# Kernel tuning notes

Hardware: AMD Instinct MI355X
Metric: run time of the kernel (lower is better)

Reference implementation:

```python
import jax, jax.numpy as jnp
import numpy as np


def setup_inputs() -> dict:
    key = jax.random.key(0)
    ks = jax.random.split(key, 5)
    B, S, H = 4, 4096, 512
    std = 1.0 / np.sqrt(H)
    x = jax.random.normal(ks[0], (B, S, H), dtype=jnp.float32)
    relative_pos = jax.random.normal(ks[1], (B, S, H), dtype=jnp.float32)
    Wq = jax.random.normal(ks[2], (H, H), dtype=jnp.float32) * std
    Wk = jax.random.normal(ks[3], (H, H), dtype=jnp.float32) * std
    Wv = jax.random.normal(ks[4], (H, H), dtype=jnp.float32) * std
    bq = jnp.zeros((H,), dtype=jnp.float32)
    bk = jnp.zeros((H,), dtype=jnp.float32)
    bv = jnp.zeros((H,), dtype=jnp.float32)
    return {"x": x, "relative_pos": relative_pos, "Wq": Wq, "bq": bq,
            "Wk": Wk, "bk": bk, "Wv": Wv, "bv": bv}


def reference(x, relative_pos, Wq, bq, Wk, bk, Wv, bv):
    H = x.shape[-1]
    scale = jnp.sqrt(jnp.asarray(H, dtype=x.dtype))
    # torch Linear: y = x @ W^T + b
    Q = jnp.einsum('bsh,oh->bso', x, Wq) + bq
    K = jnp.einsum('bsh,oh->bso', x, Wk) + bk
    V = jnp.einsum('bsh,oh->bso', x, Wv) + bv
    Kr = jnp.einsum('bsh,oh->bso', relative_pos, Wk) + bk
    # two score terms, each [B,S,S]
    scores = (jnp.einsum('bqd,bkd->bqk', Q, K) +
              jnp.einsum('bqd,bkd->bqk', Q, Kr)) / scale
    weights = jax.nn.softmax(scores, axis=-1)
    return jnp.einsum('bqk,bkd->bqd', weights, V)
```

## Files before the change

### kernel.cpp

```cpp
#include <hip/hip_runtime.h>
#include <stdint.h>

typedef __attribute__((ext_vector_type(8))) short bf16x8;
typedef __attribute__((ext_vector_type(4))) float f32x4;

#define AS1 __attribute__((address_space(1)))
#define AS3 __attribute__((address_space(3)))

__device__ __forceinline__ void gl2lds16(const void* g, void* l) {
    __builtin_amdgcn_global_load_lds((const AS1 void*)g, (AS3 void*)l, 16, 0, 0);
}

__device__ __forceinline__ unsigned short f2bf(float f) {
    uint32_t u = __builtin_bit_cast(uint32_t, f);
    uint32_t r = (u + 0x7fffu + ((u >> 16) & 1u)) >> 16;
    return (unsigned short)r;
}

constexpr int S = 4096;
constexpr int H = 512;
constexpr size_t OFF_XB  = 0;
constexpr size_t OFF_SB  = 16777216;
constexpr size_t OFF_WQB = 33554432;
constexpr size_t OFF_WKB = 34078720;
constexpr size_t OFF_WVB = 34603008;
constexpr size_t OFF_BQK = 35127296;
constexpr size_t OFF_QB  = 35131392;
constexpr size_t OFF_K2B = OFF_QB  + 16777216;
constexpr size_t OFF_VTB = OFF_K2B + 16777216;
constexpr size_t OFF_PB  = OFF_VTB + 16777216;
constexpr size_t OFF_L   = OFF_PB  + 134217728;

__global__ __launch_bounds__(256) void prep_x(const float* __restrict__ x,
                                              const float* __restrict__ rp,
                                              unsigned short* __restrict__ xb,
                                              unsigned short* __restrict__ sb) {
    const int i = (blockIdx.x * 256 + threadIdx.x) * 4;
    float4 xv = *(const float4*)(x + i);
    float4 rv = *(const float4*)(rp + i);
    uint2 xo, so;
    xo.x = (uint32_t)f2bf(xv.x) | ((uint32_t)f2bf(xv.y) << 16);
    xo.y = (uint32_t)f2bf(xv.z) | ((uint32_t)f2bf(xv.w) << 16);
    so.x = (uint32_t)f2bf(xv.x + rv.x) | ((uint32_t)f2bf(xv.y + rv.y) << 16);
    so.y = (uint32_t)f2bf(xv.z + rv.z) | ((uint32_t)f2bf(xv.w + rv.w) << 16);
    *(uint2*)(xb + i) = xo;
    *(uint2*)(sb + i) = so;
}

__global__ __launch_bounds__(256) void prep_w(const float* __restrict__ wq,
                                              const float* __restrict__ wk,
                                              const float* __restrict__ wv,
                                              const float* __restrict__ bq,
                                              const float* __restrict__ bk,
                                              unsigned short* __restrict__ wqb,
                                              unsigned short* __restrict__ wkb,
                                              unsigned short* __restrict__ wvb,
                                              float* __restrict__ bqk,
                                              float* __restrict__ lrow) {
    const int t = blockIdx.x * 256 + threadIdx.x;
    const int i = t * 4;
    float4 q = *(const float4*)(wq + i);
    float4 k = *(const float4*)(wk + i);
    float4 v = *(const float4*)(wv + i);
    uint2 o;
    o.x = (uint32_t)f2bf(q.x) | ((uint32_t)f2bf(q.y) << 16);
    o.y = (uint32_t)f2bf(q.z) | ((uint32_t)f2bf(q.w) << 16);
    *(uint2*)(wqb + i) = o;
    o.x = (uint32_t)f2bf(k.x) | ((uint32_t)f2bf(k.y) << 16);
    o.y = (uint32_t)f2bf(k.z) | ((uint32_t)f2bf(k.w) << 16);
    *(uint2*)(wkb + i) = o;
    o.x = (uint32_t)f2bf(v.x) | ((uint32_t)f2bf(v.y) << 16);
    o.y = (uint32_t)f2bf(v.z) | ((uint32_t)f2bf(v.w) << 16);
    *(uint2*)(wvb + i) = o;
    if (t < 128) {
        *(float4*)(bqk + t * 4) = *(const float4*)(bq + t * 4);
    } else if (t < 256) {
        const int u = t - 128;
        float4 b = *(const float4*)(bk + u * 4);
        *(float4*)(bqk + 512 + u * 4) = make_float4(2.f * b.x, 2.f * b.y, 2.f * b.z, 2.f * b.w);
    }
    if (t < 4096) {
        *(float4*)(lrow + t * 4) = make_float4(0.f, 0.f, 0.f, 0.f);
    }
}

template <int MODE, int SWZ, int TN, int MINW>
__global__ __launch_bounds__(256, MINW)
void gemm_bt(const unsigned short* __restrict__ Abase,
             const unsigned short* __restrict__ Bbase,
             void* __restrict__ Cbase,
             int M, int N, int K,
             long long sAz, long long sBz, long long sCz,
             const float* __restrict__ bias_n, long long sBNz,
             const float* __restrict__ bias_m,
             float scale,
             float* __restrict__ rowdiv, long long sRz)
{
    constexpr int NT = TN / 32;
    int bx = blockIdx.x, by = blockIdx.y, bz = blockIdx.z;
    if (SWZ) {
        const int gx = gridDim.x, gy = gridDim.y;
        const int id  = bx + gx * (by + gridDim.y * bz);
        const int xcd = id & 7;
        const int k   = id >> 3;
        const int kg  = k / gx;
        bx = k - kg * gx;
        const int g = xcd + 8 * kg;
        const int gz = g / gy;
        by = g - gz * gy;
        bz = gz;
    }
    const int z = bz;
    const unsigned short* A  = Abase + (size_t)z * (size_t)sAz;
    const unsigned short* Bm = Bbase + (size_t)z * (size_t)sBz;
    const int bn = bx * TN;
    const int bm = by * 128;

    constexpr int SMEM_BYTES = (MODE == 2) ? (64 * 136 * 2) : ((128 + TN) * 32 * 2);
    __shared__ __align__(16) char smem[SMEM_BYTES];
    unsigned short* As = (unsigned short*)smem;
    unsigned short* Bs = (unsigned short*)(smem + 128 * 32 * 2);

    const int tid  = threadIdx.x;
    const int wave = tid >> 6;
    const int lane = tid & 63;
    const int lm   = lane & 15;
    const int quad = lane >> 4;
    const int wm   = (wave >> 1) * 64;
    const int wn   = (wave & 1) * (TN / 2);

    const int r0 = tid >> 2;
    const int p0 = tid & 3;
    unsigned short* AsW0 = As + wave * 512;
    unsigned short* AsW1 = As + 2048 + wave * 512;
    unsigned short* BsW0 = Bs + wave * 512;
    unsigned short* BsW1 = Bs + 2048 + wave * 512;

    f32x4 acc[4][NT] = {};

    for (int k0 = 0; k0 < K; k0 += 32) {
        const unsigned short* Ap = A  + (size_t)(bm + r0) * K + k0 + p0 * 8;
        const unsigned short* Bp = Bm + (size_t)(bn + r0) * K + k0 + p0 * 8;
        __syncthreads();
        gl2lds16(Ap, AsW0);
        gl2lds16(Ap + (size_t)64 * K, AsW1);
        gl2lds16(Bp, BsW0);
        if (TN == 128) gl2lds16(Bp + (size_t)64 * K, BsW1);
        __syncthreads();

        bf16x8 af[4], bfr[NT];
        #pragma unroll
        for (int t = 0; t < 4; t++)
            af[t]  = *(const bf16x8*)(As + (wm + t * 16 + lm) * 32 + quad * 8);
        #pragma unroll
        for (int t = 0; t < NT; t++)
            bfr[t] = *(const bf16x8*)(Bs + (wn + t * 16 + lm) * 32 + quad * 8);
        #pragma unroll
        for (int mt = 0; mt < 4; mt++)
            #pragma unroll
            for (int nt = 0; nt < NT; nt++)
                acc[mt][nt] = __builtin_amdgcn_mfma_f32_16x16x32_bf16(af[mt], bfr[nt], acc[mt][nt], 0, 0, 0);
    }

    if (MODE == 0) {
        unsigned short* C = (unsigned short*)Cbase + (size_t)z * (size_t)sCz;
        const float* bn_ptr = bias_n ? bias_n + (size_t)z * (size_t)sBNz : nullptr;
        #pragma unroll
        for (int mt = 0; mt < 4; mt++) {
            #pragma unroll
            for (int i = 0; i < 4; i++) {
                const int row = bm + wm + mt * 16 + quad * 4 + i;
                const float badd = bias_m ? bias_m[row] : 0.0f;
                const size_t rb = (size_t)row * (size_t)N;
                #pragma unroll
                for (int nt = 0; nt < NT; nt++) {
                    const int col = bn + wn + nt * 16 + lm;
                    float v = acc[mt][nt][i] * scale + badd;
                    if (bn_ptr) v += bn_ptr[col];
                    C[rb + col] = f2bf(v);
                }
            }
        }
    } else if (MODE == 1) {
        float* C = (float*)Cbase + (size_t)z * (size_t)sCz;
        const float* rd = rowdiv + (size_t)z * (size_t)sRz;
        #pragma unroll
        for (int mt = 0; mt < 4; mt++) {
            #pragma unroll
            for (int i = 0; i < 4; i++) {
                const int row = bm + wm + mt * 16 + quad * 4 + i;
                const float inv = 1.0f / rd[row];
                const size_t rb = (size_t)row * (size_t)N;
                #pragma unroll
                for (int nt = 0; nt < NT; nt++) {
                    const int col = bn + wn + nt * 16 + lm;
                    C[rb + col] = acc[mt][nt][i] * inv;
                }
            }
        }
    } else {
        unsigned short* C = (unsigned short*)Cbase + (size_t)z * (size_t)sCz;
        float* lr = rowdiv + (size_t)z * (size_t)sRz;
        unsigned short* Ct = (unsigned short*)smem;
        #pragma unroll
        for (int h = 0; h < 2; h++) {
            __syncthreads();
            if ((wave >> 1) == h) {
                #pragma unroll
                for (int mt = 0; mt < 4; mt++) {
                    #pragma unroll
                    for (int i = 0; i < 4; i++) {
                        const int r = mt * 16 + quad * 4 + i;
                        const int row = bm + wm + r;
                        float rsum = 0.f;
                        #pragma unroll
                        for (int nt = 0; nt < NT; nt++) {
                            float p = __expf(acc[mt][nt][i] * scale);
                            rsum += p;
                            Ct[r * 136 + wn + nt * 16 + lm] = f2bf(p);
                        }
                        rsum += __shfl_xor(rsum, 1);
                        rsum += __shfl_xor(rsum, 2);
                        rsum += __shfl_xor(rsum, 4);
                        rsum += __shfl_xor(rsum, 8);
                        if (lm == 0) atomicAdd(lr + row, rsum);
                    }
                }
            }
            __syncthreads();
            #pragma unroll
            for (int j = 0; j < 4; j++) {
                const int r   = (tid >> 4) + 16 * j;
                const int c16 = tid & 15;
                uint4 vv = *(const uint4*)(Ct + r * 136 + c16 * 8);
                *(uint4*)(C + (size_t)(bm + 64 * h + r) * (size_t)N + bn + c16 * 8) = vv;
            }
        }
    }
}

extern "C" void kernel_launch(void* const* d_in, const int* in_sizes, int n_in,
                              void* d_out, int out_size, void* d_ws, size_t ws_size,
                              hipStream_t stream) {
    const float* x  = (const float*)d_in[0];
    const float* rp = (const float*)d_in[1];
    const float* Wq = (const float*)d_in[2];
    const float* bq = (const float*)d_in[3];
    const float* Wk = (const float*)d_in[4];
    const float* bk = (const float*)d_in[5];
    const float* Wv = (const float*)d_in[6];
    const float* bv = (const float*)d_in[7];

    char* ws = (char*)d_ws;
    unsigned short* xb  = (unsigned short*)(ws + OFF_XB);
    unsigned short* sb  = (unsigned short*)(ws + OFF_SB);
    unsigned short* wqb = (unsigned short*)(ws + OFF_WQB);
    unsigned short* wkb = (unsigned short*)(ws + OFF_WKB);
    unsigned short* wvb = (unsigned short*)(ws + OFF_WVB);
    float*          bqk = (float*)(ws + OFF_BQK);
    unsigned short* qb  = (unsigned short*)(ws + OFF_QB);
    unsigned short* k2b = (unsigned short*)(ws + OFF_K2B);
    unsigned short* vtb = (unsigned short*)(ws + OFF_VTB);
    unsigned short* pb  = (unsigned short*)(ws + OFF_PB);
    float*          lrow = (float*)(ws + OFF_L);

    prep_x<<<8192, 256, 0, stream>>>(x, rp, xb, sb);
    prep_w<<<256, 256, 0, stream>>>(Wq, Wk, Wv, bq, bk, wqb, wkb, wvb, bqk, lrow);

    gemm_bt<0, 1, 128, 2><<<dim3(4, 128, 2), 256, 0, stream>>>(
        xb, wqb, qb, 16384, 512, 512,
        8388608, 262144, 8388608,
        bqk, 512, nullptr, 1.0f, nullptr, 0);
    gemm_bt<0, 0, 128, 2><<<dim3(32, 4, 4), 256, 0, stream>>>(
        wvb, xb, vtb, 512, 4096, 512,
        0, (long long)S * H, (long long)S * H,
        nullptr, 0, bv, 1.0f, nullptr, 0);
    gemm_bt<2, 1, 128, 2><<<dim3(32, 32, 4), 256, 0, stream>>>(
        qb, k2b, pb, 4096, 4096, 512,
        (long long)S * H, (long long)S * H, (long long)S * S,
        nullptr, 0, nullptr, 0.044194173824159216f,
        lrow, 4096);
    gemm_bt<1, 1, 64, 4><<<dim3(8, 32, 4), 256, 0, stream>>>(
        pb, vtb, d_out, 4096, 512, 4096,
        (long long)S * S, (long long)S * H, (long long)S * H,
        nullptr, 0, nullptr, 1.0f, lrow, 4096);
}
```

Measured before the change: 407.5 us.

## Use BK=64 K-tiles, fixed 128x128 tiles, single-pass softmax epilogue

The GEMM main loop now stages two 32-wide K slices per iteration (BK=64), which halves the number of barrier pairs per K. The TN/MINW template parameters are removed, so every GEMM uses 128x128 tiles. The P·V GEMM grid shrinks from 8 to 4 column blocks and its occupancy hint drops from 4 to 2. The exp/score epilogue writes the full 128-row tile to LDS in one pass instead of two halves, and the score GEMM turns off XCD swizzling. These changes cost more LDS per block and may lower occupancy and parallelism for the P·V GEMM.

```diff
diff --git a/kernel.cpp b/kernel.cpp
--- a/kernel.cpp
+++ b/kernel.cpp
@@ -84,8 +84,8 @@
     }
 }
 
-template <int MODE, int SWZ, int TN, int MINW>
-__global__ __launch_bounds__(256, MINW)
+template <int MODE, int SWZ>
+__global__ __launch_bounds__(256, 2)
 void gemm_bt(const unsigned short* __restrict__ Abase,
              const unsigned short* __restrict__ Bbase,
              void* __restrict__ Cbase,
@@ -96,7 +96,6 @@
              float scale,
              float* __restrict__ rowdiv, long long sRz)
 {
-    constexpr int NT = TN / 32;
     int bx = blockIdx.x, by = blockIdx.y, bz = blockIdx.z;
     if (SWZ) {
         const int gx = gridDim.x, gy = gridDim.y;
@@ -113,13 +112,13 @@
     const int z = bz;
     const unsigned short* A  = Abase + (size_t)z * (size_t)sAz;
     const unsigned short* Bm = Bbase + (size_t)z * (size_t)sBz;
-    const int bn = bx * TN;
+    const int bn = bx * 128;
     const int bm = by * 128;
 
-    constexpr int SMEM_BYTES = (MODE == 2) ? (64 * 136 * 2) : ((128 + TN) * 32 * 2);
+    constexpr int SMEM_BYTES = (MODE == 2) ? (128 * 136 * 2) : (4 * 4096 * 2);
     __shared__ __align__(16) char smem[SMEM_BYTES];
     unsigned short* As = (unsigned short*)smem;
-    unsigned short* Bs = (unsigned short*)(smem + 128 * 32 * 2);
+    unsigned short* Bs = (unsigned short*)(smem + 16384);
 
     const int tid  = threadIdx.x;
     const int wave = tid >> 6;
@@ -127,39 +126,43 @@
     const int lm   = lane & 15;
     const int quad = lane >> 4;
     const int wm   = (wave >> 1) * 64;
-    const int wn   = (wave & 1) * (TN / 2);
+    const int wn   = (wave & 1) * 64;
 
     const int r0 = tid >> 2;
     const int p0 = tid & 3;
-    unsigned short* AsW0 = As + wave * 512;
-    unsigned short* AsW1 = As + 2048 + wave * 512;
-    unsigned short* BsW0 = Bs + wave * 512;
-    unsigned short* BsW1 = Bs + 2048 + wave * 512;
-
-    f32x4 acc[4][NT] = {};
-
-    for (int k0 = 0; k0 < K; k0 += 32) {
-        const unsigned short* Ap = A  + (size_t)(bm + r0) * K + k0 + p0 * 8;
-        const unsigned short* Bp = Bm + (size_t)(bn + r0) * K + k0 + p0 * 8;
-        __syncthreads();
-        gl2lds16(Ap, AsW0);
-        gl2lds16(Ap + (size_t)64 * K, AsW1);
-        gl2lds16(Bp, BsW0);
-        if (TN == 128) gl2lds16(Bp + (size_t)64 * K, BsW1);
-        __syncthreads();
-
-        bf16x8 af[4], bfr[NT];
-        #pragma unroll
-        for (int t = 0; t < 4; t++)
-            af[t]  = *(const bf16x8*)(As + (wm + t * 16 + lm) * 32 + quad * 8);
-        #pragma unroll
-        for (int t = 0; t < NT; t++)
-            bfr[t] = *(const bf16x8*)(Bs + (wn + t * 16 + lm) * 32 + quad * 8);
-        #pragma unroll
-        for (int mt = 0; mt < 4; mt++)
-            #pragma unroll
-            for (int nt = 0; nt < NT; nt++)
-                acc[mt][nt] = __builtin_amdgcn_mfma_f32_16x16x32_bf16(af[mt], bfr[nt], acc[mt][nt], 0, 0, 0);
+
+    f32x4 acc[4][4] = {};
+
+    for (int k0 = 0; k0 < K; k0 += 64) {
+        __syncthreads();
+        #pragma unroll
+        for (int pp = 0; pp < 2; pp++) {
+            const unsigned short* Ap = A  + (size_t)(bm + r0) * K + k0 + pp * 32 + p0 * 8;
+            const unsigned short* Bp = Bm + (size_t)(bn + r0) * K + k0 + pp * 32 + p0 * 8;
+            unsigned short* Asp = As + pp * 4096;
+            unsigned short* Bsp = Bs + pp * 4096;
+            gl2lds16(Ap,                    Asp + wave * 512);
+            gl2lds16(Ap + (size_t)64 * K,   Asp + 2048 + wave * 512);
+            gl2lds16(Bp,                    Bsp + wave * 512);
+            gl2lds16(Bp + (size_t)64 * K,   Bsp + 2048 + wave * 512);
+        }
+        __syncthreads();
+
+        #pragma unroll
+        for (int pp = 0; pp < 2; pp++) {
+            bf16x8 af[4], bfr[4];
+            #pragma unroll
+            for (int t = 0; t < 4; t++)
+                af[t]  = *(const bf16x8*)(As + pp * 4096 + (wm + t * 16 + lm) * 32 + quad * 8);
+            #pragma unroll
+            for (int t = 0; t < 4; t++)
+                bfr[t] = *(const bf16x8*)(Bs + pp * 4096 + (wn + t * 16 + lm) * 32 + quad * 8);
+            #pragma unroll
+            for (int mt = 0; mt < 4; mt++)
+                #pragma unroll
+                for (int nt = 0; nt < 4; nt++)
+                    acc[mt][nt] = __builtin_amdgcn_mfma_f32_16x16x32_bf16(af[mt], bfr[nt], acc[mt][nt], 0, 0, 0);
+        }
     }
 
     if (MODE == 0) {
@@ -173,7 +176,7 @@
                 const float badd = bias_m ? bias_m[row] : 0.0f;
                 const size_t rb = (size_t)row * (size_t)N;
                 #pragma unroll
-                for (int nt = 0; nt < NT; nt++) {
+                for (int nt = 0; nt < 4; nt++) {
                     const int col = bn + wn + nt * 16 + lm;
                     float v = acc[mt][nt][i] * scale + badd;
                     if (bn_ptr) v += bn_ptr[col];
@@ -192,7 +195,7 @@
                 const float inv = 1.0f / rd[row];
                 const size_t rb = (size_t)row * (size_t)N;
                 #pragma unroll
-                for (int nt = 0; nt < NT; nt++) {
+                for (int nt = 0; nt < 4; nt++) {
                     const int col = bn + wn + nt * 16 + lm;
                     C[rb + col] = acc[mt][nt][i] * inv;
                 }
@@ -202,39 +205,33 @@
         unsigned short* C = (unsigned short*)Cbase + (size_t)z * (size_t)sCz;
         float* lr = rowdiv + (size_t)z * (size_t)sRz;
         unsigned short* Ct = (unsigned short*)smem;
-        #pragma unroll
-        for (int h = 0; h < 2; h++) {
-            __syncthreads();
-            if ((wave >> 1) == h) {
-                #pragma unroll
-                for (int mt = 0; mt < 4; mt++) {
-                    #pragma unroll
-                    for (int i = 0; i < 4; i++) {
-                        const int r = mt * 16 + quad * 4 + i;
-                        const int row = bm + wm + r;
-                        float rsum = 0.f;
-                        #pragma unroll
-                        for (int nt = 0; nt < NT; nt++) {
-                            float p = __expf(acc[mt][nt][i] * scale);
-                            rsum += p;
-                            Ct[r * 136 + wn + nt * 16 + lm] = f2bf(p);
-                        }
-                        rsum += __shfl_xor(rsum, 1);
-                        rsum += __shfl_xor(rsum, 2);
-                        rsum += __shfl_xor(rsum, 4);
-                        rsum += __shfl_xor(rsum, 8);
-                        if (lm == 0) atomicAdd(lr + row, rsum);
-                    }
+        __syncthreads();
+        #pragma unroll
+        for (int mt = 0; mt < 4; mt++) {
+            #pragma unroll
+            for (int i = 0; i < 4; i++) {
+                const int r = wm + mt * 16 + quad * 4 + i;
+                float rsum = 0.f;
+                #pragma unroll
+                for (int nt = 0; nt < 4; nt++) {
+                    float p = __expf(acc[mt][nt][i] * scale);
+                    rsum += p;
+                    Ct[r * 136 + wn + nt * 16 + lm] = f2bf(p);
                 }
+                rsum += __shfl_xor(rsum, 1);
+                rsum += __shfl_xor(rsum, 2);
+                rsum += __shfl_xor(rsum, 4);
+                rsum += __shfl_xor(rsum, 8);
+                if (lm == 0) atomicAdd(lr + bm + r, rsum);
             }
-            __syncthreads();
-            #pragma unroll
-            for (int j = 0; j < 4; j++) {
-                const int r   = (tid >> 4) + 16 * j;
-                const int c16 = tid & 15;
-                uint4 vv = *(const uint4*)(Ct + r * 136 + c16 * 8);
-                *(uint4*)(C + (size_t)(bm + 64 * h + r) * (size_t)N + bn + c16 * 8) = vv;
-            }
+        }
+        __syncthreads();
+        #pragma unroll
+        for (int j = 0; j < 8; j++) {
+            const int r   = (tid >> 4) + 16 * j;
+            const int c16 = tid & 15;
+            uint4 vv = *(const uint4*)(Ct + r * 136 + c16 * 8);
+            *(uint4*)(C + (size_t)(bm + r) * (size_t)N + bn + c16 * 8) = vv;
         }
     }
 }
@@ -267,20 +264,20 @@
     prep_x<<<8192, 256, 0, stream>>>(x, rp, xb, sb);
     prep_w<<<256, 256, 0, stream>>>(Wq, Wk, Wv, bq, bk, wqb, wkb, wvb, bqk, lrow);
 
-    gemm_bt<0, 1, 128, 2><<<dim3(4, 128, 2), 256, 0, stream>>>(
+    gemm_bt<0, 1><<<dim3(4, 128, 2), 256, 0, stream>>>(
         xb, wqb, qb, 16384, 512, 512,
         8388608, 262144, 8388608,
         bqk, 512, nullptr, 1.0f, nullptr, 0);
-    gemm_bt<0, 0, 128, 2><<<dim3(32, 4, 4), 256, 0, stream>>>(
+    gemm_bt<0, 0><<<dim3(32, 4, 4), 256, 0, stream>>>(
         wvb, xb, vtb, 512, 4096, 512,
         0, (long long)S * H, (long long)S * H,
         nullptr, 0, bv, 1.0f, nullptr, 0);
-    gemm_bt<2, 1, 128, 2><<<dim3(32, 32, 4), 256, 0, stream>>>(
+    gemm_bt<2, 0><<<dim3(32, 32, 4), 256, 0, stream>>>(
         qb, k2b, pb, 4096, 4096, 512,
         (long long)S * H, (long long)S * H, (long long)S * S,
         nullptr, 0, nullptr, 0.044194173824159216f,
         lrow, 4096);
-    gemm_bt<1, 1, 64, 4><<<dim3(8, 32, 4), 256, 0, stream>>>(
+    gemm_bt<1, 1><<<dim3(4, 32, 4), 256, 0, stream>>>(
         pb, vtb, d_out, 4096, 512, 4096,
         (long long)S * S, (long long)S * H, (long long)S * H,
         nullptr, 0, nullptr, 1.0f, lrow, 4096);
```

Result: faster. 347.5 us (-14.7%).
